# Kernel tuning notes

Hardware: AMD Instinct MI355X
Metric: run time of the kernel (lower is better)

The kernel has to match this reference:

```python
import jax, jax.numpy as jnp
import numpy as np
from jax import lax

NCLASSES = 3
NMS_PRE = 100
NMS_THR = 0.01
SCORE_THR = 0.1
MAX_NUM = 50
H, W = 248, 216
BS = 16


def make_anchors():
    # Faithful to Anchors(ranges, sizes, rotations) in __init__.
    z0s = np.array([-0.6, -0.6, -1.78], np.float32)
    sizes = np.array([[0.6, 0.8, 1.73], [0.6, 1.76, 1.73], [1.6, 3.9, 1.56]], np.float32)
    rotations = np.array([0.0, 1.57], np.float32)
    x = (np.arange(W, dtype=np.float32) + 0.5) * (69.12 / W)
    y = (np.arange(H, dtype=np.float32) + 0.5) * (79.36 / H) - 39.68
    yy, xx = np.meshgrid(y, x, indexing='ij')  # (H, W)
    anchors = np.zeros((H, W, 3, 2, 7), np.float32)
    for c in range(3):
        for r in range(2):
            anchors[:, :, c, r, 0] = xx
            anchors[:, :, c, r, 1] = yy
            anchors[:, :, c, r, 2] = z0s[c]
            anchors[:, :, c, r, 3:6] = sizes[c]
            anchors[:, :, c, r, 6] = rotations[r]
    return jnp.asarray(anchors)


def setup_inputs() -> dict:
    key = jax.random.key(0)
    k1, k2, k3 = jax.random.split(key, 3)
    return {
        'bbox_cls_pred': jax.random.normal(k1, (BS, 18, H, W), jnp.float32),
        'bbox_pred': jax.random.normal(k2, (BS, 42, H, W), jnp.float32) * 0.1,
        'bbox_dir_cls_pred': jax.random.normal(k3, (BS, 12, H, W), jnp.float32),
        'anchors': make_anchors(),
    }


def limit_period(val, offset=1.0, period=np.pi):
    return val - jnp.floor(val / period + offset) * period


def anchors2bboxes(anchors, deltas):
    xa, ya, za, wa, la, ha, ra = [anchors[:, i] for i in range(7)]
    dx, dy, dz, dw, dl, dh, dr = [deltas[:, i] for i in range(7)]
    da = jnp.sqrt(wa * wa + la * la)
    x = dx * da + xa
    y = dy * da + ya
    z = dz * ha + za + ha * 0.5
    w = wa * jnp.exp(dw)
    l = la * jnp.exp(dl)
    h = ha * jnp.exp(dh)
    z = z - h * 0.5
    theta = ra + dr
    return jnp.stack([x, y, z, w, l, h, theta], axis=-1)


def nms_keep(boxes2d, scores, valid, thresh):
    # Greedy NMS over fixed NMS_PRE boxes; invalid boxes never kept / never suppress.
    n = scores.shape[0]
    order = jnp.argsort(-jnp.where(valid, scores, -jnp.inf))
    b = boxes2d[order]
    v = valid[order]
    area = (b[:, 2] - b[:, 0]) * (b[:, 3] - b[:, 1])
    x1 = jnp.maximum(b[:, None, 0], b[None, :, 0])
    y1 = jnp.maximum(b[:, None, 1], b[None, :, 1])
    x2 = jnp.minimum(b[:, None, 2], b[None, :, 2])
    y2 = jnp.minimum(b[:, None, 3], b[None, :, 3])
    inter = jnp.maximum(x2 - x1, 0.0) * jnp.maximum(y2 - y1, 0.0)
    iou = inter / (area[:, None] + area[None, :] - inter + 1e-8)
    idx = jnp.arange(n)
    def body(i, keep):
        sup = (iou[i] > thresh) & (idx > i) & keep[i]
        return keep & ~sup
    keep = lax.fori_loop(0, n, body, v)
    return jnp.zeros(n, bool).at[order].set(keep)


def process_single(cls_pred, box_pred, dir_pred, anchors):
    # cls_pred (18,H,W), box_pred (42,H,W), dir_pred (12,H,W), anchors (H,W,3,2,7)
    cls = jnp.transpose(cls_pred, (1, 2, 0)).reshape(-1, NCLASSES)
    box = jnp.transpose(box_pred, (1, 2, 0)).reshape(-1, 7)
    dirp = jnp.transpose(dir_pred, (1, 2, 0)).reshape(-1, 2)
    anc = anchors.reshape(-1, 7)
    cls = jax.nn.sigmoid(cls)
    dir_cls = jnp.argmax(dirp, axis=1)
    _, inds = lax.top_k(jnp.max(cls, axis=1), NMS_PRE)
    cls = cls[inds]
    box = box[inds]
    dir_cls = dir_cls[inds]
    anc = anc[inds]
    bboxes = anchors2bboxes(anc, box)  # (NMS_PRE, 7): x,y,z,w,l,h,theta
    xy = bboxes[:, :2]
    wl = bboxes[:, 3:5]
    boxes2d = jnp.concatenate([xy - wl / 2, xy + wl / 2], axis=-1)
    # Torch code detaches theta through limit_period; dir term is constant.
    theta = lax.stop_gradient(limit_period(bboxes[:, 6])) + (1.0 - dir_cls.astype(bboxes.dtype)) * np.pi
    bboxes = bboxes.at[:, 6].set(theta)
    keeps = []
    for c in range(NCLASSES):
        sc = cls[:, c]
        valid = sc > SCORE_THR
        keeps.append(nms_keep(boxes2d, sc, valid, NMS_THR) & valid)
    keep = jnp.stack(keeps)            # (3, NMS_PRE)
    scores_all = cls.T                 # (3, NMS_PRE)
    flat = jnp.where(keep, scores_all, -1.0).reshape(-1)
    final_scores, fi = lax.top_k(flat, MAX_NUM)
    sel = fi % NMS_PRE
    labels = fi // NMS_PRE
    out_bboxes = bboxes[sel]
    mask = final_scores > 0.0
    return out_bboxes, labels, final_scores, mask


def reference(bbox_cls_pred, bbox_pred, bbox_dir_cls_pred, anchors):
    f = jax.vmap(process_single, in_axes=(0, 0, 0, None))
    return f(bbox_cls_pred, bbox_pred, bbox_dir_cls_pred, anchors)
```

## Files before the change

kernel.cpp:

```cpp
#include <hip/hip_runtime.h>
#include <cstdint>

#pragma clang fp contract(off)

#define HH 248
#define WW 216
#define HW (HH*WW)
#define NROW (6*HW)
#define BATCH 16
#define NPRE 100
#define MAXNUM 50
#define NB 2048
#define CAP 2048
#define SBLK 53
#define K0 64
#define PIF 3.14159274101257324f

#define T0BKT 1966u

#define CNTB_OFF 0
#define KEYS_OFF 3584
#define SH_OFF   (KEYS_OFF + BATCH*SBLK*K0*8)

__device__ __forceinline__ float sigmoidf_ref(float x) {
    if (x >= 0.0f) {
        return 1.0f / (1.0f + expf(-x));
    } else {
        float e = expf(x);
        return e / (1.0f + e);
    }
}

__device__ __forceinline__ unsigned bucket_of(unsigned bits) {
    unsigned b = (bits >= 0x3F000000u) ? (1024u + ((bits - 0x3F000000u) >> 13))
                                       : (bits >> 20);
    return (b > (unsigned)(NB - 1)) ? (unsigned)(NB - 1) : b;
}

__device__ __forceinline__ void emit_one(unsigned bits, unsigned row,
                                         unsigned* hist, unsigned* lcnt,
                                         unsigned long long* kseg) {
    unsigned bk = bucket_of(bits);
    atomicAdd(&hist[bk], 1u);
    if (bk >= T0BKT) {
        unsigned pos = atomicAdd(lcnt, 1u);
        if (pos < (unsigned)K0)
            kseg[pos] = ((unsigned long long)bits << 32) |
                        (unsigned long long)(0xFFFFFFFFu - row);
    }
}

__global__ __launch_bounds__(256) void k_score(const float* __restrict__ cls,
                                               unsigned short* __restrict__ subhist,
                                               unsigned* __restrict__ cntB,
                                               unsigned long long* __restrict__ keys) {
    int t = threadIdx.x, blk = blockIdx.x, b = blockIdx.y;
    __shared__ unsigned hist[NB];
    __shared__ unsigned lcnt;
    for (int i = t; i < NB; i += 256) hist[i] = 0;
    if (t == 0) lcnt = 0;
    __syncthreads();

    unsigned long long* kseg = keys + (size_t)(b * SBLK + blk) * K0;
    int cell0 = blk * 1024 + t * 4;
    if (cell0 < HW) {
        const float* p = cls + (size_t)b * 18 * HW;
        #pragma unroll
        for (int a = 0; a < 6; ++a) {
            float4 l0 = *(const float4*)(p + (size_t)(a*3+0)*HW + cell0);
            float4 l1 = *(const float4*)(p + (size_t)(a*3+1)*HW + cell0);
            float4 l2 = *(const float4*)(p + (size_t)(a*3+2)*HW + cell0);
            unsigned b0 = __float_as_uint(sigmoidf_ref(fmaxf(l0.x, fmaxf(l1.x, l2.x))));
            unsigned b1 = __float_as_uint(sigmoidf_ref(fmaxf(l0.y, fmaxf(l1.y, l2.y))));
            unsigned b2 = __float_as_uint(sigmoidf_ref(fmaxf(l0.z, fmaxf(l1.z, l2.z))));
            unsigned b3 = __float_as_uint(sigmoidf_ref(fmaxf(l0.w, fmaxf(l1.w, l2.w))));
            emit_one(b0, (unsigned)((cell0+0)*6 + a), hist, &lcnt, kseg);
            emit_one(b1, (unsigned)((cell0+1)*6 + a), hist, &lcnt, kseg);
            emit_one(b2, (unsigned)((cell0+2)*6 + a), hist, &lcnt, kseg);
            emit_one(b3, (unsigned)((cell0+3)*6 + a), hist, &lcnt, kseg);
        }
    }
    __syncthreads();
    unsigned short* sh = subhist + (size_t)(b * SBLK + blk) * NB;
    for (int i = t; i < NB; i += 256) sh[i] = (unsigned short)hist[i];
    if (t == 0) cntB[b * SBLK + blk] = lcnt;
}

__global__ __launch_bounds__(256) void k_final(
    const float* __restrict__ cls, const float* __restrict__ box,
    const float* __restrict__ dir, const float* __restrict__ anc,
    const unsigned* __restrict__ cntB, const unsigned long long* __restrict__ keys,
    const unsigned short* __restrict__ subhist,
    float* __restrict__ out) {
    int b = blockIdx.x, t = threadIdx.x;

    __shared__ unsigned long long keyS[CAP];
    __shared__ int   selRow[NPRE];
    __shared__ float bb[NPRE][7];
    __shared__ float b2d[NPRE][4];
    __shared__ float areaS[NPRE];
    __shared__ float clsS[3][NPRE];
    __shared__ float svalS[3][NPRE];
    __shared__ int   ordS[3][NPRE];
    __shared__ int   rankS[3][NPRE];
    __shared__ float4 sbox[3][NPRE];
    __shared__ float  sarea[3][NPRE];
    __shared__ unsigned keepInit[3][4];
    __shared__ unsigned long long maskS[3][NPRE][2];
    __shared__ unsigned long long keepBits[3][2];
    __shared__ float flatS[3*NPRE];
    __shared__ unsigned hq[256];
    __shared__ unsigned cntS[SBLK];
    __shared__ int  pref[SBLK + 1];
    __shared__ int  tbS;
    __shared__ unsigned cumS;
    __shared__ int  safeS;
    __shared__ unsigned mcnt;

    if (t == 0) { tbS = -1; cumS = 0; mcnt = 0; }
    if (t < SBLK) cntS[t] = cntB[b * SBLK + t];
    __syncthreads();
    {
        const unsigned short* base = subhist + (size_t)b * SBLK * NB;
        for (int c0 = NB - 256; c0 >= 0; c0 -= 256) {
            unsigned s = 0;
            #pragma unroll
            for (int k = 0; k < SBLK; ++k) s += base[(size_t)k * NB + (c0 + t)];
            hq[t] = s;
            __syncthreads();
            if (t == 0) {
                unsigned cum = cumS;
                for (int j = 255; j >= 0; --j) {
                    cum += hq[j];
                    if (cum >= NPRE) { tbS = c0 + j; break; }
                }
                cumS = cum;
            }
            __syncthreads();
            if (tbS >= 0) break;
        }
    }
    int tb = (tbS < 0) ? 0 : tbS;

    if (t == 0) {
        int ok = (tb >= (int)T0BKT) ? 1 : 0;
        int s = 0;
        #pragma unroll 4
        for (int k = 0; k < SBLK; ++k) {
            unsigned c = cntS[k];
            if (c > (unsigned)K0) ok = 0;
            pref[k] = s;
            s += (int)((c < (unsigned)K0) ? c : (unsigned)K0);
        }
        pref[SBLK] = s;
        if (s > CAP || s < NPRE) ok = 0;
        safeS = ok;
    }
    __syncthreads();

    int M;
    if (safeS) {
        for (int k = 0; k < SBLK; ++k) {
            int c = (int)cntS[k];
            for (int i = t; i < c; i += 256) {
                unsigned long long key = keys[(size_t)(b * SBLK + k) * K0 + i];
                if (bucket_of((unsigned)(key >> 32)) >= (unsigned)tb) {
                    unsigned pos = atomicAdd(&mcnt, 1u);
                    keyS[pos] = key;
                }
            }
        }
        __syncthreads();
        M = (int)mcnt;
    } else {
        const float* p = cls + (size_t)b * 18 * HW;
        for (int cell = t; cell < HW; cell += 256) {
            for (int a = 0; a < 6; ++a) {
                float v0 = p[(size_t)(a*3+0)*HW + cell];
                float v1 = p[(size_t)(a*3+1)*HW + cell];
                float v2 = p[(size_t)(a*3+2)*HW + cell];
                unsigned bits = __float_as_uint(sigmoidf_ref(fmaxf(v0, fmaxf(v1, v2))));
                if (bucket_of(bits) >= (unsigned)tb) {
                    unsigned pos = atomicAdd(&mcnt, 1u);
                    if (pos < (unsigned)CAP)
                        keyS[pos] = ((unsigned long long)bits << 32) |
                                    (unsigned long long)(0xFFFFFFFFu - (unsigned)(cell*6 + a));
                }
            }
        }
        __syncthreads();
        M = (mcnt < (unsigned)CAP) ? (int)mcnt : CAP;
    }
    __syncthreads();

    for (int i = t; i < M; i += 256) {
        unsigned long long k = keyS[i];
        int r = 0;
        int j = 0;
        for (; j + 3 < M; j += 4) {
            unsigned long long a0 = keyS[j+0], a1 = keyS[j+1];
            unsigned long long a2 = keyS[j+2], a3 = keyS[j+3];
            r += (int)(a0 > k) + (int)(a1 > k) + (int)(a2 > k) + (int)(a3 > k);
        }
        for (; j < M; ++j) r += (int)(keyS[j] > k);
        if (r < NPRE) selRow[r] = (int)(0xFFFFFFFFu - (unsigned)(k & 0xFFFFFFFFull));
    }
    __syncthreads();

    if (t < NPRE) {
        int row = selRow[t];
        int a = row % 6;
        int cell = row / 6;
        const float* cb = cls + (size_t)b * 18 * HW + cell;
        clsS[0][t] = sigmoidf_ref(cb[(size_t)(a*3+0)*HW]);
        clsS[1][t] = sigmoidf_ref(cb[(size_t)(a*3+1)*HW]);
        clsS[2][t] = sigmoidf_ref(cb[(size_t)(a*3+2)*HW]);
        const float* db = dir + (size_t)b * 12 * HW + cell;
        float d0 = db[(size_t)(a*2+0)*HW];
        float d1 = db[(size_t)(a*2+1)*HW];
        int dircls = (d1 > d0) ? 1 : 0;
        const float* pb = box + (size_t)b * 42 * HW + cell;
        float dx = pb[(size_t)(a*7+0)*HW], dy = pb[(size_t)(a*7+1)*HW], dz = pb[(size_t)(a*7+2)*HW];
        float dw = pb[(size_t)(a*7+3)*HW], dl = pb[(size_t)(a*7+4)*HW], dh = pb[(size_t)(a*7+5)*HW];
        float dr = pb[(size_t)(a*7+6)*HW];
        const float* ab = anc + (size_t)row * 7;
        float xa = ab[0], ya = ab[1], za = ab[2];
        float wa = ab[3], la = ab[4], ha = ab[5], ra = ab[6];
        float da = sqrtf(wa*wa + la*la);
        float x = dx*da + xa;
        float y = dy*da + ya;
        float z = dz*ha + za + ha*0.5f;
        float wv = wa*expf(dw);
        float lv = la*expf(dl);
        float hv = ha*expf(dh);
        z = z - hv*0.5f;
        float th0 = ra + dr;
        float lim = th0 - floorf(th0/PIF + 1.0f)*PIF;
        float theta = lim + (1.0f - (float)dircls)*PIF;
        bb[t][0]=x; bb[t][1]=y; bb[t][2]=z; bb[t][3]=wv; bb[t][4]=lv; bb[t][5]=hv; bb[t][6]=theta;
        b2d[t][0] = x - wv*0.5f;
        b2d[t][1] = y - lv*0.5f;
        b2d[t][2] = x + wv*0.5f;
        b2d[t][3] = y + lv*0.5f;
        areaS[t] = (b2d[t][2]-b2d[t][0]) * (b2d[t][3]-b2d[t][1]);
    }
    if (t < 12) keepInit[t/4][t%4] = 0u;
    __syncthreads();

    for (int w = t; w < 3*NPRE; w += 256) {
        int c = w / NPRE, p = w % NPRE;
        float sc = clsS[c][p];
        svalS[c][p] = (sc > 0.1f) ? sc : -INFINITY;
    }
    __syncthreads();

    for (int w = t; w < 3*NPRE; w += 256) {
        int c = w / NPRE, p = w % NPRE;
        float v = svalS[c][p];
        int r = 0;
        #pragma unroll
        for (int j0 = 0; j0 < NPRE; j0 += 4) {
            float v0 = svalS[c][j0+0], v1 = svalS[c][j0+1];
            float v2 = svalS[c][j0+2], v3 = svalS[c][j0+3];
            r += (int)(v0 > v || (v0 == v && (j0+0) < p));
            r += (int)(v1 > v || (v1 == v && (j0+1) < p));
            r += (int)(v2 > v || (v2 == v && (j0+2) < p));
            r += (int)(v3 > v || (v3 == v && (j0+3) < p));
        }
        ordS[c][r] = p;
        rankS[c][p] = r;
        if (v != -INFINITY) atomicOr(&keepInit[c][r >> 5], 1u << (r & 31));
    }
    __syncthreads();

    for (int w = t; w < 3*NPRE; w += 256) {
        int c = w / NPRE, i = w % NPRE;
        int pi = ordS[c][i];
        sbox[c][i] = make_float4(b2d[pi][0], b2d[pi][1], b2d[pi][2], b2d[pi][3]);
        sarea[c][i] = areaS[pi];
    }
    __syncthreads();

    for (int w = t; w < 3*NPRE; w += 256) {
        int c = w / NPRE, i = w % NPRE;
        float4 bi = sbox[c][i];
        float ai = sarea[c][i];
        unsigned long long m0 = 0ULL, m1 = 0ULL;
        #pragma unroll 2
        for (int j = i + 1; j < NPRE; ++j) {
            float4 bj = sbox[c][j];
            float x1 = fmaxf(bi.x, bj.x);
            float y1 = fmaxf(bi.y, bj.y);
            float x2 = fminf(bi.z, bj.z);
            float y2 = fminf(bi.w, bj.w);
            float inter = fmaxf(x2 - x1, 0.0f) * fmaxf(y2 - y1, 0.0f);
            float iou = inter / (ai + sarea[c][j] - inter + 1e-8f);
            unsigned long long hit = (iou > 0.01f) ? 1ULL : 0ULL;
            if (j < 64) m0 |= hit << j;
            else        m1 |= hit << (j - 64);
        }
        maskS[c][i][0] = m0;
        maskS[c][i][1] = m1;
    }
    __syncthreads();

    if (t < 3) {
        int c = t;
        unsigned long long k0 = (unsigned long long)keepInit[c][0] |
                                ((unsigned long long)keepInit[c][1] << 32);
        unsigned long long k1 = (unsigned long long)keepInit[c][2] |
                                ((unsigned long long)keepInit[c][3] << 32);
        for (int i = 0; i < NPRE; ++i) {
            unsigned long long bit = (i < 64) ? (k0 >> i) : (k1 >> (i - 64));
            if (bit & 1ULL) {
                k0 &= ~maskS[c][i][0];
                k1 &= ~maskS[c][i][1];
            }
        }
        keepBits[c][0] = k0;
        keepBits[c][1] = k1;
    }
    __syncthreads();

    for (int w = t; w < 3*NPRE; w += 256) {
        int c = w / NPRE, p = w % NPRE;
        int r = rankS[c][p];
        unsigned long long bit = (r < 64) ? (keepBits[c][0] >> r) : (keepBits[c][1] >> (r - 64));
        flatS[w] = (bit & 1ULL) ? clsS[c][p] : -1.0f;
    }
    __syncthreads();

    for (int i = t; i < 3*NPRE; i += 256) {
        float vi = flatS[i];
        int r2 = 0;
        #pragma unroll
        for (int j0 = 0; j0 < 3*NPRE; j0 += 4) {
            float v0 = flatS[j0+0], v1 = flatS[j0+1];
            float v2 = flatS[j0+2], v3 = flatS[j0+3];
            r2 += (int)(v0 > vi || (v0 == vi && (j0+0) < i));
            r2 += (int)(v1 > vi || (v1 == vi && (j0+1) < i));
            r2 += (int)(v2 > vi || (v2 == vi && (j0+2) < i));
            r2 += (int)(v3 > vi || (v3 == vi && (j0+3) < i));
        }
        if (r2 < MAXNUM) {
            int p = i % NPRE;
            int lab = i / NPRE;
            int o = b * MAXNUM + r2;
            float* ob = out + (size_t)o * 7;
            for (int j = 0; j < 7; ++j) ob[j] = bb[p][j];
            out[BATCH*MAXNUM*7 + o] = (float)lab;
            out[BATCH*MAXNUM*8 + o] = vi;
            out[BATCH*MAXNUM*9 + o] = (vi > 0.0f) ? 1.0f : 0.0f;
        }
    }
}

extern "C" void kernel_launch(void* const* d_in, const int* in_sizes, int n_in,
                              void* d_out, int out_size, void* d_ws, size_t ws_size,
                              hipStream_t stream) {
    const float* cls = (const float*)d_in[0];
    const float* box = (const float*)d_in[1];
    const float* dir = (const float*)d_in[2];
    const float* anc = (const float*)d_in[3];
    float* out = (float*)d_out;
    char* ws = (char*)d_ws;

    unsigned* cntB = (unsigned*)(ws + CNTB_OFF);
    unsigned long long* keys = (unsigned long long*)(ws + KEYS_OFF);
    unsigned short* subhist  = (unsigned short*)(ws + SH_OFF);

    dim3 g(SBLK, BATCH);
    k_score<<<g, 256, 0, stream>>>(cls, subhist, cntB, keys);
    k_final<<<BATCH, 256, 0, stream>>>(cls, box, dir, anc, cntB, keys, subhist, out);
}
```

Before: 315.1 us.

## Parallelize threshold histogram scan, prefetch candidate keys, and skip suppressed NMS rows

Replaces the single-thread backward cumulative scan over histogram buckets with a wave-shuffle plus cross-wave suffix sum, so all 256 threads find the threshold bucket together. Candidate keys are loaded into registers before the histogram scan so their global latency overlaps it. The serial greedy NMS loop now visits only surviving boxes using count-trailing-zeros iteration. The safety check moves to a ballot, and full unrolling is dropped on two rank loops. Costs are higher register pressure from the 14-entry key array, and the changed safety condition (bounded by the threshold count rather than summed slot counts) must still guarantee correctness.

After: 297.8 us. -5.5%, faster.

```diff
diff --git a/kernel.cpp b/kernel.cpp
--- a/kernel.cpp
+++ b/kernel.cpp
@@ -14,6 +14,8 @@
 #define CAP 2048
 #define SBLK 53
 #define K0 64
+#define NSLOT (SBLK*K0)
+#define QMAX 14
 #define PIF 3.14159274101257324f
 
 #define T0BKT 1966u
@@ -110,64 +112,80 @@
     __shared__ unsigned long long keepBits[3][2];
     __shared__ float flatS[3*NPRE];
     __shared__ unsigned hq[256];
+    __shared__ unsigned wq[4];
     __shared__ unsigned cntS[SBLK];
-    __shared__ int  pref[SBLK + 1];
     __shared__ int  tbS;
-    __shared__ unsigned cumS;
+    __shared__ unsigned StbS;
     __shared__ int  safeS;
     __shared__ unsigned mcnt;
 
-    if (t == 0) { tbS = -1; cumS = 0; mcnt = 0; }
+    if (t == 0) { tbS = -1; StbS = 0; mcnt = 0; }
     if (t < SBLK) cntS[t] = cntB[b * SBLK + t];
     __syncthreads();
+
+    unsigned long long kq[QMAX];
+    #pragma unroll
+    for (int q = 0; q < QMAX; ++q) {
+        unsigned long long kk = 0ULL;
+        int s = t + q * 256;
+        if (s < NSLOT) {
+            int k = s >> 6, i = s & 63;
+            if ((unsigned)i < cntS[k])
+                kk = keys[(size_t)(b * SBLK + k) * K0 + i];
+        }
+        kq[q] = kk;
+    }
+
     {
         const unsigned short* base = subhist + (size_t)b * SBLK * NB;
+        unsigned carry = 0;
         for (int c0 = NB - 256; c0 >= 0; c0 -= 256) {
             unsigned s = 0;
+            #pragma unroll 4
+            for (int k = 0; k < SBLK; ++k) s += base[(size_t)k * NB + (c0 + t)];
+            unsigned val = s;
+            int lane = t & 63;
             #pragma unroll
-            for (int k = 0; k < SBLK; ++k) s += base[(size_t)k * NB + (c0 + t)];
-            hq[t] = s;
+            for (int d = 1; d < 64; d <<= 1) {
+                unsigned y = __shfl_down(val, d, 64);
+                if (lane + d < 64) val += y;
+            }
+            if (lane == 0) wq[t >> 6] = val;
             __syncthreads();
-            if (t == 0) {
-                unsigned cum = cumS;
-                for (int j = 255; j >= 0; --j) {
-                    cum += hq[j];
-                    if (cum >= NPRE) { tbS = c0 + j; break; }
-                }
-                cumS = cum;
+            unsigned tail = 0;
+            for (int w2 = (t >> 6) + 1; w2 < 4; ++w2) tail += wq[w2];
+            unsigned S = val + tail + carry;
+            hq[t] = S;
+            __syncthreads();
+            unsigned Snext = (t < 255) ? hq[t + 1] : carry;
+            if (S >= (unsigned)NPRE && Snext < (unsigned)NPRE) {
+                tbS = c0 + t;
+                StbS = S;
             }
             __syncthreads();
             if (tbS >= 0) break;
+            carry = hq[0];
         }
     }
     int tb = (tbS < 0) ? 0 : tbS;
 
-    if (t == 0) {
-        int ok = (tb >= (int)T0BKT) ? 1 : 0;
-        int s = 0;
-        #pragma unroll 4
-        for (int k = 0; k < SBLK; ++k) {
-            unsigned c = cntS[k];
-            if (c > (unsigned)K0) ok = 0;
-            pref[k] = s;
-            s += (int)((c < (unsigned)K0) ? c : (unsigned)K0);
-        }
-        pref[SBLK] = s;
-        if (s > CAP || s < NPRE) ok = 0;
-        safeS = ok;
+    if (t < 64) {
+        unsigned c = (t < SBLK) ? cntS[t] : 0u;
+        unsigned long long ov = __ballot(c > (unsigned)K0);
+        if (t == 0)
+            safeS = (tbS >= (int)T0BKT) && (ov == 0ULL) &&
+                    (StbS <= (unsigned)CAP) ? 1 : 0;
     }
     __syncthreads();
 
     int M;
     if (safeS) {
-        for (int k = 0; k < SBLK; ++k) {
-            int c = (int)cntS[k];
-            for (int i = t; i < c; i += 256) {
-                unsigned long long key = keys[(size_t)(b * SBLK + k) * K0 + i];
-                if (bucket_of((unsigned)(key >> 32)) >= (unsigned)tb) {
-                    unsigned pos = atomicAdd(&mcnt, 1u);
-                    keyS[pos] = key;
-                }
+        #pragma unroll
+        for (int q = 0; q < QMAX; ++q) {
+            unsigned long long kk = kq[q];
+            if (bucket_of((unsigned)(kk >> 32)) >= (unsigned)tb) {
+                unsigned pos = atomicAdd(&mcnt, 1u);
+                keyS[pos] = kk;
             }
         }
         __syncthreads();
@@ -258,7 +276,6 @@
         int c = w / NPRE, p = w % NPRE;
         float v = svalS[c][p];
         int r = 0;
-        #pragma unroll
         for (int j0 = 0; j0 < NPRE; j0 += 4) {
             float v0 = svalS[c][j0+0], v1 = svalS[c][j0+1];
             float v2 = svalS[c][j0+2], v3 = svalS[c][j0+3];
@@ -310,12 +327,21 @@
                                 ((unsigned long long)keepInit[c][1] << 32);
         unsigned long long k1 = (unsigned long long)keepInit[c][2] |
                                 ((unsigned long long)keepInit[c][3] << 32);
-        for (int i = 0; i < NPRE; ++i) {
-            unsigned long long bit = (i < 64) ? (k0 >> i) : (k1 >> (i - 64));
-            if (bit & 1ULL) {
-                k0 &= ~maskS[c][i][0];
-                k1 &= ~maskS[c][i][1];
-            }
+        unsigned long long todo = k0;
+        while (todo) {
+            int i = __builtin_ctzll(todo);
+            unsigned long long m0 = maskS[c][i][0];
+            unsigned long long m1 = maskS[c][i][1];
+            k0 &= ~m0;
+            k1 &= ~m1;
+            todo = (todo & (todo - 1)) & ~m0;
+        }
+        todo = k1;
+        while (todo) {
+            int i = __builtin_ctzll(todo);
+            unsigned long long m1 = maskS[c][64 + i][1];
+            k1 &= ~m1;
+            todo = (todo & (todo - 1)) & ~m1;
         }
         keepBits[c][0] = k0;
         keepBits[c][1] = k1;
@@ -333,7 +359,6 @@
     for (int i = t; i < 3*NPRE; i += 256) {
         float vi = flatS[i];
         int r2 = 0;
-        #pragma unroll
         for (int j0 = 0; j0 < 3*NPRE; j0 += 4) {
             float v0 = flatS[j0+0], v1 = flatS[j0+1];
             float v2 = flatS[j0+2], v3 = flatS[j0+3];
```
